# Performance work log

Measured on AMD Instinct MI355X. Metric: run time of the kernel, lower is better.

Reference implementation:

```python
import jax, jax.numpy as jnp
import numpy as np

B, T, V, LSRC, D = 4, 128, 50257, 512, 512
PAD_ID = 0
GAMMA1, GAMMA2 = 1.0, 0.1
BETA, MAX_ITER = 2.0, 400


def setup_inputs() -> dict:
    key = jax.random.key(0)
    ks = jax.random.split(key, 7)
    # output_mle are per-token probabilities (original takes torch.log of them)
    output_mle = jax.random.uniform(ks[0], (B, T, V), jnp.float32, 1e-4, 1.0)
    attn_dist = jax.random.uniform(ks[1], (B, LSRC, T), jnp.float32)
    coverage = jax.random.uniform(ks[2], (B, LSRC, T), jnp.float32)
    trg = jax.random.randint(ks[3], (B, T), 0, V)
    dec_mask = jax.random.randint(ks[4], (B, T), 0, 2).astype(bool)
    dec_len = jax.random.randint(ks[5], (B,), 1, T)
    W_emb = jax.random.normal(ks[6], (V, D), jnp.float32) * 0.02
    return {"output_mle": output_mle, "attn_dist": attn_dist, "coverage": coverage,
            "trg": trg, "dec_mask": dec_mask, "dec_len": dec_len, "W_emb": W_emb}


def ipot(a1, a2, beta=BETA, max_iter=MAX_ITER):
    # a1, a2: [n, d_hid] (already flattened from [B, T, d_hid])
    n = a1.shape[0]
    a1n = a1 / jnp.linalg.norm(a1, axis=1, keepdims=True)
    a2n = a2 / jnp.linalg.norm(a2, axis=1, keepdims=True)
    C = a1n @ a2n.T                      # [n, n] cosine cost
    A = jnp.exp(-C / beta)
    eye = jnp.eye(n, dtype=C.dtype)
    sigma0 = jnp.full((n, 1), 1.0 / n, C.dtype)
    T0 = jnp.full((n, n), 1.0 / (n * n), C.dtype)

    def step(carry, _):
        Tm, sigma = carry
        Q = A * Tm
        dvec = 1.0 / n / (Q @ sigma)          # [n, 1]
        sigma = 1.0 / n / (Q.T @ dvec)        # [n, 1]
        # Faithful to torch source: diag(d) * Q * diag(sigma) is ELEMENTWISE,
        # so only the diagonal of the product survives.
        Tm = dvec * Q * sigma.T * eye
        return (Tm, sigma), None

    (Tm, _), _ = jax.lax.scan(step, (T0, sigma0), None, length=max_iter)
    return jnp.sum(Tm * C)


def reference(output_mle, attn_dist, coverage, trg, dec_mask, dec_len, W_emb):
    # --- NLL loss (Eq. 6): mean -log p[target] over non-pad tokens ---
    logp = jnp.log(output_mle)
    tok_lp = jnp.take_along_axis(logp, trg[..., None], axis=-1)[..., 0]   # [B, T]
    valid = (trg != PAD_ID)
    nll = -jnp.sum(jnp.where(valid, tok_lp, 0.0)) / jnp.sum(valid).astype(logp.dtype)

    # --- Coverage loss (Eq. 12) ---
    cov = jnp.sum(jnp.minimum(attn_dist, coverage), axis=1)               # [B, T]
    cov = jnp.where(dec_mask, 0.0, cov)
    cov_loss = jnp.sum(cov) / jnp.sum(dec_len).astype(cov.dtype)

    # --- OT loss via IPOT ---
    trg_emb = W_emb[trg]                                                  # [B, T, D]
    probs = jax.nn.softmax(output_mle, axis=-1)
    pred = jnp.einsum('btv,vd->btd', probs, W_emb)                        # [B, T, D]
    ot = ipot(pred.reshape(-1, D), trg_emb.reshape(-1, D))

    # Faithful to source: gamma2 added as a constant (not multiplied by ot)
    return nll + GAMMA1 * cov_loss + GAMMA2 + ot
```

## Files before the change

### kernel.cpp

```cpp
#include <hip/hip_runtime.h>
#include <math.h>

#define B_ 4
#define T_ 128
#define V_ 50257
#define D_ 512
#define NROWS 512
#define GAMMA2_ 0.1f

#define BK 32
#define KC 1600
#define SPLITK 32
#define NIT (KC / BK)
#define LDA 40
#define LDB 40

#define SLICE (NROWS * D_)

typedef __attribute__((ext_vector_type(8))) short s8v;
typedef __attribute__((ext_vector_type(4))) float f4v;

#define WS_PART_OFF 1024

__device__ inline unsigned int pack2bf(float f0, float f1) {
    unsigned int u0 = __float_as_uint(f0);
    unsigned int u1 = __float_as_uint(f1);
    u0 += 0x7fffu + ((u0 >> 16) & 1u);
    u1 += 0x7fffu + ((u1 >> 16) & 1u);
    return (u0 >> 16) | (u1 & 0xffff0000u);
}

__device__ inline void sync_lds() {
    __builtin_amdgcn_s_waitcnt(0xC07F);
    __builtin_amdgcn_s_barrier();
}

__device__ inline float wave_reduce(float v) {
    #pragma unroll
    for (int o = 32; o > 0; o >>= 1) v += __shfl_down(v, o, 64);
    return v;
}

__global__ void misc_kernel(const float* __restrict__ output_mle,
                            const float* __restrict__ attn,
                            const float* __restrict__ cover,
                            const int* __restrict__ trg,
                            const int* __restrict__ dec_mask,
                            const int* __restrict__ dec_len,
                            float* __restrict__ acc) {
    int bid = blockIdx.x;
    if (bid < 64) {
        float s = 0.f;
        const float4* a4 = (const float4*)attn;
        const float4* c4 = (const float4*)cover;
        for (int i4 = bid * 256 + threadIdx.x; i4 < 65536; i4 += 64 * 256) {
            float4 a = a4[i4];
            float4 c = c4[i4];
            int b = i4 >> 14;
            int t = (i4 << 2) & (T_ - 1);
            int4 m = *(const int4*)&dec_mask[(b << 7) + t];
            s += m.x ? 0.f : fminf(a.x, c.x);
            s += m.y ? 0.f : fminf(a.y, c.y);
            s += m.z ? 0.f : fminf(a.z, c.z);
            s += m.w ? 0.f : fminf(a.w, c.w);
        }
        s = wave_reduce(s);
        if ((threadIdx.x & 63) == 0) atomicAdd(&acc[2], s);
    } else {
        float lp = 0.f, cnt = 0.f;
        for (int i = threadIdx.x; i < NROWS; i += 256) {
            int tg = trg[i];
            if (tg != 0) {
                lp += __logf(output_mle[(size_t)i * V_ + tg]);
                cnt += 1.f;
            }
        }
        lp = wave_reduce(lp); cnt = wave_reduce(cnt);
        if ((threadIdx.x & 63) == 0) { atomicAdd(&acc[0], lp); atomicAdd(&acc[1], cnt); }
        if (threadIdx.x < B_) atomicAdd(&acc[3], (float)dec_len[threadIdx.x]);
    }
}

__launch_bounds__(256)
__global__ void gemm_kernel(const float* __restrict__ X,
                            const float* __restrict__ W,
                            float* __restrict__ part,
                            int use_atomic) {
    __shared__ __align__(16) short As[128 * LDA];
    __shared__ __align__(16) short Bs[128 * LDB];

    const int bx   = blockIdx.x;
    const int tile = bx & 15;
    const int s    = bx >> 4;
    const int i0   = (tile & 3) * 128;
    const int d0   = (tile >> 2) * 128;
    const int ks   = s * KC;
    const int ke   = min(ks + KC, V_);

    const int tid  = threadIdx.x;
    const int lane = tid & 63;
    const int wave = tid >> 6;
    const int wm   = (wave & 1) * 64;
    const int wn   = (wave >> 1) * 64;
    const int l15  = lane & 15;
    const int l4   = lane >> 4;

    const int ar   = tid >> 1;
    const int akh  = (tid & 1) * 16;
    const int bn2  = (tid & 63) * 2;
    const int bkq  = (tid >> 6) * 8;

    f4v acc[4][4];
    #pragma unroll
    for (int a = 0; a < 4; a++)
        #pragma unroll
        for (int b = 0; b < 4; b++) acc[a][b] = (f4v)0.f;

    auto stageA = [&](const float4 (&ab)[4]) {
        const float* f = (const float*)&ab[0];
        unsigned int au[8];
        #pragma unroll
        for (int p = 0; p < 8; p++)
            au[p] = pack2bf(__expf(f[2 * p]), __expf(f[2 * p + 1]));
        *(uint4*)&As[ar * LDA + akh]     = *(const uint4*)&au[0];
        *(uint4*)&As[ar * LDA + akh + 8] = *(const uint4*)&au[4];
    };
    auto stageB = [&](const float2 (&bb)[8]) {
        unsigned int r0[4], r1[4];
        #pragma unroll
        for (int p = 0; p < 4; p++) {
            r0[p] = pack2bf(bb[2 * p].x, bb[2 * p + 1].x);
            r1[p] = pack2bf(bb[2 * p].y, bb[2 * p + 1].y);
        }
        *(uint4*)&Bs[bn2 * LDB + bkq]       = *(const uint4*)&r0[0];
        *(uint4*)&Bs[(bn2 + 1) * LDB + bkq] = *(const uint4*)&r1[0];
    };
    auto domfma = [&]() {
        s8v af[4], bfr[4];
        #pragma unroll
        for (int mi = 0; mi < 4; mi++)
            af[mi] = *(const s8v*)&As[(wm + mi * 16 + l15) * LDA + l4 * 8];
        #pragma unroll
        for (int ni = 0; ni < 4; ni++)
            bfr[ni] = *(const s8v*)&Bs[(wn + ni * 16 + l15) * LDB + l4 * 8];
        #pragma unroll
        for (int mi = 0; mi < 4; mi++)
            #pragma unroll
            for (int ni = 0; ni < 4; ni++)
                acc[mi][ni] = __builtin_amdgcn_mfma_f32_16x16x32_bf16(
                    af[mi], bfr[ni], acc[mi][ni], 0, 0, 0);
    };
    auto issue = [&](float4 (&ab)[4], float2 (&bb)[8], const float* ap, const float* bp) {
        #pragma unroll
        for (int q = 0; q < 4; q++) ab[q] = *(const float4*)(ap + q * 4);
        #pragma unroll
        for (int j = 0; j < 8; j++) bb[j] = *(const float2*)(bp + (size_t)j * D_);
    };

    if (ks + KC <= V_) {
        const float* ap = X + (size_t)(i0 + ar) * V_ + ks + akh;
        const float* bp = W + d0 + bn2 + (size_t)(ks + bkq) * D_;
        float4 a0[4], a1[4];
        float2 b0[8], b1[8];
        issue(a0, b0, ap, bp);
        #pragma unroll 1
        for (int it = 0; it < NIT; it += 2) {
            ap += BK; bp += (size_t)BK * D_;
            if (it + 1 < NIT) issue(a1, b1, ap, bp);
            sync_lds();
            stageA(a0); stageB(b0);
            sync_lds();
            domfma();

            ap += BK; bp += (size_t)BK * D_;
            if (it + 2 < NIT) issue(a0, b0, ap, bp);
            sync_lds();
            stageA(a1); stageB(b1);
            sync_lds();
            domfma();
        }
    } else {
        const float* Abase = X + (size_t)(i0 + ar) * V_;
        const float* Bbase = W + d0 + bn2;
        for (int k0 = ks; k0 < ke; k0 += BK) {
            float4 ab[4];
            float2 bb[8];
            #pragma unroll
            for (int q = 0; q < 4; q++) {
                int gk = min(k0 + akh + q * 4, V_ - 4);
                ab[q] = *(const float4*)(Abase + gk);
            }
            #pragma unroll
            for (int j = 0; j < 8; j++) {
                int gk = min(k0 + bkq + j, V_ - 1);
                bb[j] = *(const float2*)(Bbase + (size_t)gk * D_);
            }
            sync_lds();
            {
                unsigned int au[8];
                const float* f = (const float*)&ab[0];
                #pragma unroll
                for (int p = 0; p < 8; p++) {
                    int g0 = k0 + akh + 2 * p;
                    float e0 = (g0     < ke) ? __expf(f[2 * p])     : 0.f;
                    float e1 = (g0 + 1 < ke) ? __expf(f[2 * p + 1]) : 0.f;
                    au[p] = pack2bf(e0, e1);
                }
                *(uint4*)&As[ar * LDA + akh]     = *(const uint4*)&au[0];
                *(uint4*)&As[ar * LDA + akh + 8] = *(const uint4*)&au[4];
            }
            {
                unsigned int r0[4], r1[4];
                #pragma unroll
                for (int p = 0; p < 4; p++) {
                    int g0 = k0 + bkq + 2 * p;
                    float x0 = (g0     < ke) ? bb[2 * p].x     : 0.f;
                    float x1 = (g0 + 1 < ke) ? bb[2 * p + 1].x : 0.f;
                    float y0 = (g0     < ke) ? bb[2 * p].y     : 0.f;
                    float y1 = (g0 + 1 < ke) ? bb[2 * p + 1].y : 0.f;
                    r0[p] = pack2bf(x0, x1);
                    r1[p] = pack2bf(y0, y1);
                }
                *(uint4*)&Bs[bn2 * LDB + bkq]       = *(const uint4*)&r0[0];
                *(uint4*)&Bs[(bn2 + 1) * LDB + bkq] = *(const uint4*)&r1[0];
            }
            sync_lds();
            domfma();
        }
    }

    float* dst = part + (use_atomic ? 0 : (size_t)s * SLICE);
    #pragma unroll
    for (int mi = 0; mi < 4; mi++) {
        #pragma unroll
        for (int ni = 0; ni < 4; ni++) {
            int col = d0 + wn + ni * 16 + l15;
            #pragma unroll
            for (int r = 0; r < 4; r++) {
                int row = i0 + wm + mi * 16 + l4 * 4 + r;
                if (use_atomic) atomicAdd(&dst[row * D_ + col], acc[mi][ni][r]);
                else            dst[row * D_ + col] = acc[mi][ni][r];
            }
        }
    }
}

__global__ void ot_kernel(const float* __restrict__ part,
                          const float* __restrict__ W,
                          const int* __restrict__ trg,
                          float* __restrict__ acc,
                          int nsl) {
    int wave = threadIdx.x >> 6, lane = threadIdx.x & 63;
    int row  = blockIdx.x * 4 + wave;
    const size_t off = (size_t)row * D_ + lane * 8;

    float4 p0 = {0, 0, 0, 0}, p1 = {0, 0, 0, 0};
    for (int s = 0; s < nsl; s++) {
        const float4* ps = (const float4*)(part + (size_t)s * SLICE + off);
        float4 q0 = ps[0], q1 = ps[1];
        p0.x += q0.x; p0.y += q0.y; p0.z += q0.z; p0.w += q0.w;
        p1.x += q1.x; p1.y += q1.y; p1.z += q1.z; p1.w += q1.w;
    }
    const float4* t4 = (const float4*)(W + (size_t)trg[row] * D_ + lane * 8);
    float4 t0 = t4[0], t1 = t4[1];

    float dot = p0.x * t0.x + p0.y * t0.y + p0.z * t0.z + p0.w * t0.w
              + p1.x * t1.x + p1.y * t1.y + p1.z * t1.z + p1.w * t1.w;
    float nn  = p0.x * p0.x + p0.y * p0.y + p0.z * p0.z + p0.w * p0.w
              + p1.x * p1.x + p1.y * p1.y + p1.z * p1.z + p1.w * p1.w;
    float tt  = t0.x * t0.x + t0.y * t0.y + t0.z * t0.z + t0.w * t0.w
              + t1.x * t1.x + t1.y * t1.y + t1.z * t1.z + t1.w * t1.w;

    dot = wave_reduce(dot); nn = wave_reduce(nn); tt = wave_reduce(tt);
    if (lane == 0)
        atomicAdd(&acc[4], (dot / sqrtf(nn * tt)) * (1.0f / (float)NROWS));
}

__global__ void finalize_kernel(const float* __restrict__ acc, float* __restrict__ out) {
    if (threadIdx.x == 0)
        out[0] = -acc[0] / acc[1] + acc[2] / acc[3] + GAMMA2_ + acc[4];
}

extern "C" void kernel_launch(void* const* d_in, const int* in_sizes, int n_in,
                              void* d_out, int out_size, void* d_ws, size_t ws_size,
                              hipStream_t stream) {
    const float* output_mle = (const float*)d_in[0];
    const float* attn       = (const float*)d_in[1];
    const float* cover      = (const float*)d_in[2];
    const int*   trg        = (const int*)d_in[3];
    const int*   dec_mask   = (const int*)d_in[4];
    const int*   dec_len    = (const int*)d_in[5];
    const float* W          = (const float*)d_in[6];
    float* out  = (float*)d_out;
    float* acc  = (float*)d_ws;
    float* part = acc + WS_PART_OFF;

    const size_t need = (size_t)WS_PART_OFF * 4 + (size_t)SPLITK * SLICE * 4;
    const bool partial = (ws_size >= need);

    if (partial) {
        hipMemsetAsync(d_ws, 0, WS_PART_OFF * sizeof(float), stream);
    } else {
        hipMemsetAsync(d_ws, 0, (WS_PART_OFF + SLICE) * sizeof(float), stream);
    }
    misc_kernel<<<65, 256, 0, stream>>>(output_mle, attn, cover, trg, dec_mask, dec_len, acc);
    gemm_kernel<<<16 * SPLITK, 256, 0, stream>>>(output_mle, W, part, partial ? 0 : 1);
    ot_kernel<<<NROWS / 4, 256, 0, stream>>>(part, W, trg, acc, partial ? SPLITK : 1);
    finalize_kernel<<<1, 64, 0, stream>>>(acc, out);
}
```

Measured before the change: 322.0 us.

## Pre-convert exp(X) and transposed W to bf16 buffers, then run a direct-to-LDS GEMM

Adds a prep kernel that computes exp of the probabilities and packs them to bf16 in a padded buffer, transposes W into a bf16 K-major buffer, and folds in the misc (NLL/coverage) work. A new GEMM uses global_load_lds to move the bf16 tiles straight into LDS and runs with a 48-way K split. The aim is to remove fp32 loads and in-loop conversion from the GEMM inner loop. In exchange it adds a large extra write and reread of bf16 copies (~50MB each) and needs a much larger workspace, falling back to the old path otherwise.

```diff
diff --git a/kernel.cpp b/kernel.cpp
--- a/kernel.cpp
+++ b/kernel.cpp
@@ -14,13 +14,22 @@
 #define NIT (KC / BK)
 #define LDA 40
 #define LDB 40
-
 #define SLICE (NROWS * D_)
+#define WS_PART_OFF 1024
+
+#define SPLITK2 48
+#define KC2 1056
+#define KP 50688
+#define NXB 2048
+#define NWB ((KP / 64) * (D_ / 64))
+#define ACC_BYTES 4096
+#define XB_BYTES ((size_t)NROWS * KP * 2)
+#define WT_BYTES ((size_t)D_ * KP * 2)
+#define PART2_BYTES ((size_t)SPLITK2 * SLICE * 4)
+#define NEED_NEW (ACC_BYTES + XB_BYTES + WT_BYTES + PART2_BYTES)
 
 typedef __attribute__((ext_vector_type(8))) short s8v;
 typedef __attribute__((ext_vector_type(4))) float f4v;
-
-#define WS_PART_OFF 1024
 
 __device__ inline unsigned int pack2bf(float f0, float f1) {
     unsigned int u0 = __float_as_uint(f0);
@@ -41,14 +50,20 @@
     return v;
 }
 
-__global__ void misc_kernel(const float* __restrict__ output_mle,
-                            const float* __restrict__ attn,
-                            const float* __restrict__ cover,
-                            const int* __restrict__ trg,
-                            const int* __restrict__ dec_mask,
-                            const int* __restrict__ dec_len,
-                            float* __restrict__ acc) {
-    int bid = blockIdx.x;
+__device__ __forceinline__ void gload16(const unsigned short* g, unsigned short* l) {
+    __builtin_amdgcn_global_load_lds(
+        (const __attribute__((address_space(1))) unsigned int*)g,
+        (__attribute__((address_space(3))) unsigned int*)l, 16, 0, 0);
+}
+
+__device__ void misc_body(int bid,
+                          const float* __restrict__ output_mle,
+                          const float* __restrict__ attn,
+                          const float* __restrict__ cover,
+                          const int* __restrict__ trg,
+                          const int* __restrict__ dec_mask,
+                          const int* __restrict__ dec_len,
+                          float* __restrict__ acc) {
     if (bid < 64) {
         float s = 0.f;
         const float4* a4 = (const float4*)attn;
@@ -81,6 +96,159 @@
     }
 }
 
+__global__ void misc_kernel(const float* __restrict__ output_mle,
+                            const float* __restrict__ attn,
+                            const float* __restrict__ cover,
+                            const int* __restrict__ trg,
+                            const int* __restrict__ dec_mask,
+                            const int* __restrict__ dec_len,
+                            float* __restrict__ acc) {
+    misc_body(blockIdx.x, output_mle, attn, cover, trg, dec_mask, dec_len, acc);
+}
+
+__launch_bounds__(256)
+__global__ void prep_kernel(const float* __restrict__ X,
+                            const float* __restrict__ W,
+                            const float* __restrict__ attn,
+                            const float* __restrict__ cover,
+                            const int* __restrict__ trg,
+                            const int* __restrict__ dec_mask,
+                            const int* __restrict__ dec_len,
+                            float* __restrict__ acc,
+                            unsigned short* __restrict__ Xb,
+                            unsigned short* __restrict__ Wt) {
+    const int bid = blockIdx.x;
+    const int tid = threadIdx.x;
+    if (bid < NXB) {
+        const int upr = KP / 8;
+        for (int u = bid * 256 + tid; u < NROWS * upr; u += NXB * 256) {
+            int row = u / upr;
+            int k8  = (u - row * upr) * 8;
+            const float* src = X + (size_t)row * V_ + k8;
+            unsigned int pk[4];
+            if (k8 + 8 <= V_) {
+                float e[8];
+                #pragma unroll
+                for (int j = 0; j < 8; j++) e[j] = __expf(src[j]);
+                #pragma unroll
+                for (int p = 0; p < 4; p++) pk[p] = pack2bf(e[2 * p], e[2 * p + 1]);
+            } else {
+                #pragma unroll
+                for (int p = 0; p < 4; p++) {
+                    float e0 = (k8 + 2 * p     < V_) ? __expf(src[2 * p])     : 0.f;
+                    float e1 = (k8 + 2 * p + 1 < V_) ? __expf(src[2 * p + 1]) : 0.f;
+                    pk[p] = pack2bf(e0, e1);
+                }
+            }
+            *(uint4*)&Xb[(size_t)row * KP + k8] = *(uint4*)pk;
+        }
+    } else if (bid < NXB + NWB) {
+        __shared__ float Ls[64][64];
+        int w  = bid - NXB;
+        int kt = w >> 3;
+        int dt = w & 7;
+        int k0 = kt << 6, d0 = dt << 6;
+        int r0 = tid >> 4;
+        int c0 = (tid & 15) << 2;
+        #pragma unroll
+        for (int q = 0; q < 4; q++) {
+            int r  = (q << 4) + r0;
+            int gk = k0 + r;
+            float4 v;
+            if (gk < V_) v = *(const float4*)&W[(size_t)gk * D_ + d0 + c0];
+            else         v = make_float4(0.f, 0.f, 0.f, 0.f);
+            *(float4*)&Ls[r][c0] = v;
+        }
+        __syncthreads();
+        int d  = tid >> 2;
+        int kc = (tid & 3) << 4;
+        unsigned int pk[8];
+        #pragma unroll
+        for (int p = 0; p < 8; p++)
+            pk[p] = pack2bf(Ls[kc + 2 * p][d], Ls[kc + 2 * p + 1][d]);
+        unsigned short* dst = Wt + (size_t)(d0 + d) * KP + k0 + kc;
+        *(uint4*)&dst[0] = *(uint4*)&pk[0];
+        *(uint4*)&dst[8] = *(uint4*)&pk[4];
+    } else {
+        misc_body(bid - (NXB + NWB), X, attn, cover, trg, dec_mask, dec_len, acc);
+    }
+}
+
+__launch_bounds__(256)
+__global__ void gemm2_kernel(const unsigned short* __restrict__ Xb,
+                             const unsigned short* __restrict__ Wt,
+                             float* __restrict__ part) {
+    __shared__ __align__(16) unsigned short As[128 * 32];
+    __shared__ __align__(16) unsigned short Bs[128 * 32];
+
+    const int bx   = blockIdx.x;
+    const int tile = bx & 15;
+    const int s    = bx >> 4;
+    const int i0   = (tile & 3) * 128;
+    const int d0   = (tile >> 2) * 128;
+    const size_t ks = (size_t)s * KC2;
+
+    const int tid  = threadIdx.x;
+    const int lane = tid & 63;
+    const int wave = tid >> 6;
+    const int wm   = (wave & 1) * 64;
+    const int wn   = (wave >> 1) * 64;
+    const int l15  = lane & 15;
+    const int l4   = lane >> 4;
+
+    const int grow = wave * 16 + (lane >> 2);
+    const int gk8  = (lane & 3) * 8;
+    const unsigned short* gA0 = Xb + (size_t)(i0 + grow) * KP + ks + gk8;
+    const unsigned short* gA1 = gA0 + (size_t)64 * KP;
+    const unsigned short* gB0 = Wt + (size_t)(d0 + grow) * KP + ks + gk8;
+    const unsigned short* gB1 = gB0 + (size_t)64 * KP;
+    unsigned short* lA = As + wave * 512;
+    unsigned short* lB = Bs + wave * 512;
+
+    f4v acc[4][4];
+    #pragma unroll
+    for (int a = 0; a < 4; a++)
+        #pragma unroll
+        for (int b = 0; b < 4; b++) acc[a][b] = (f4v)0.f;
+
+    #pragma unroll 1
+    for (int kk = 0; kk < KC2; kk += 32) {
+        __syncthreads();
+        gload16(gA0 + kk, lA);
+        gload16(gA1 + kk, lA + 2048);
+        gload16(gB0 + kk, lB);
+        gload16(gB1 + kk, lB + 2048);
+        __syncthreads();
+        s8v af[4], bfr[4];
+        #pragma unroll
+        for (int mi = 0; mi < 4; mi++)
+            af[mi] = *(const s8v*)&As[(wm + mi * 16 + l15) * 32 + l4 * 8];
+        #pragma unroll
+        for (int ni = 0; ni < 4; ni++)
+            bfr[ni] = *(const s8v*)&Bs[(wn + ni * 16 + l15) * 32 + l4 * 8];
+        #pragma unroll
+        for (int mi = 0; mi < 4; mi++)
+            #pragma unroll
+            for (int ni = 0; ni < 4; ni++)
+                acc[mi][ni] = __builtin_amdgcn_mfma_f32_16x16x32_bf16(
+                    af[mi], bfr[ni], acc[mi][ni], 0, 0, 0);
+    }
+
+    float* dst = part + (size_t)s * SLICE;
+    #pragma unroll
+    for (int mi = 0; mi < 4; mi++) {
+        #pragma unroll
+        for (int ni = 0; ni < 4; ni++) {
+            int col = d0 + wn + ni * 16 + l15;
+            #pragma unroll
+            for (int r = 0; r < 4; r++) {
+                int row = i0 + wm + mi * 16 + l4 * 4 + r;
+                dst[row * D_ + col] = acc[mi][ni][r];
+            }
+        }
+    }
+}
+
 __launch_bounds__(256)
 __global__ void gemm_kernel(const float* __restrict__ X,
                             const float* __restrict__ W,
@@ -293,18 +461,31 @@
     const float* W          = (const float*)d_in[6];
     float* out  = (float*)d_out;
     float* acc  = (float*)d_ws;
-    float* part = acc + WS_PART_OFF;
-
-    const size_t need = (size_t)WS_PART_OFF * 4 + (size_t)SPLITK * SLICE * 4;
-    const bool partial = (ws_size >= need);
-
-    if (partial) {
-        hipMemsetAsync(d_ws, 0, WS_PART_OFF * sizeof(float), stream);
+
+    const bool newpath = (ws_size >= NEED_NEW);
+
+    if (newpath) {
+        unsigned short* Xb = (unsigned short*)((char*)d_ws + ACC_BYTES);
+        unsigned short* Wt = (unsigned short*)((char*)d_ws + ACC_BYTES + XB_BYTES);
+        float* part2 = (float*)((char*)d_ws + ACC_BYTES + XB_BYTES + WT_BYTES);
+        hipMemsetAsync(d_ws, 0, ACC_BYTES, stream);
+        prep_kernel<<<NXB + NWB + 65, 256, 0, stream>>>(
+            output_mle, W, attn, cover, trg, dec_mask, dec_len, acc, Xb, Wt);
+        gemm2_kernel<<<16 * SPLITK2, 256, 0, stream>>>(Xb, Wt, part2);
+        ot_kernel<<<NROWS / 4, 256, 0, stream>>>(part2, W, trg, acc, SPLITK2);
+        finalize_kernel<<<1, 64, 0, stream>>>(acc, out);
     } else {
-        hipMemsetAsync(d_ws, 0, (WS_PART_OFF + SLICE) * sizeof(float), stream);
-    }
-    misc_kernel<<<65, 256, 0, stream>>>(output_mle, attn, cover, trg, dec_mask, dec_len, acc);
-    gemm_kernel<<<16 * SPLITK, 256, 0, stream>>>(output_mle, W, part, partial ? 0 : 1);
-    ot_kernel<<<NROWS / 4, 256, 0, stream>>>(part, W, trg, acc, partial ? SPLITK : 1);
-    finalize_kernel<<<1, 64, 0, stream>>>(acc, out);
-}
+        float* part = acc + WS_PART_OFF;
+        const size_t need = (size_t)WS_PART_OFF * 4 + (size_t)SPLITK * SLICE * 4;
+        const bool partial = (ws_size >= need);
+        if (partial) {
+            hipMemsetAsync(d_ws, 0, WS_PART_OFF * sizeof(float), stream);
+        } else {
+            hipMemsetAsync(d_ws, 0, (WS_PART_OFF + SLICE) * sizeof(float), stream);
+        }
+        misc_kernel<<<65, 256, 0, stream>>>(output_mle, attn, cover, trg, dec_mask, dec_len, acc);
+        gemm_kernel<<<16 * SPLITK, 256, 0, stream>>>(output_mle, W, part, partial ? 0 : 1);
+        ot_kernel<<<NROWS / 4, 256, 0, stream>>>(part, W, trg, acc, partial ? SPLITK : 1);
+        finalize_kernel<<<1, 64, 0, stream>>>(acc, out);
+    }
+}
```

After: 331.0 us. 1.03x slower.

## Group GEMM split-K blocks by XCD and parallelize OT partial reduction

Applied to the files above, without the earlier changes.

Remaps GEMM block indices so that all 16 output tiles sharing one K-slice land on the same XCD, letting them share the W slice in that XCD's L2. The OT kernel now uses one block per row, with four waves each summing a quarter of the split-K partials; the wave results are combined through shared memory. This aims to cut L2 misses in the GEMM and raise memory-level parallelism in the partial-sum reduction. The cost is 4x more OT blocks plus an extra LDS barrier.

```diff
diff --git a/kernel.cpp b/kernel.cpp
--- a/kernel.cpp
+++ b/kernel.cpp
@@ -90,8 +90,10 @@
     __shared__ __align__(16) short Bs[128 * LDB];
 
     const int bx   = blockIdx.x;
-    const int tile = bx & 15;
-    const int s    = bx >> 4;
+    const int xcd  = bx & 7;
+    const int j    = bx >> 3;
+    const int s    = xcd + 8 * (j >> 4);
+    const int tile = j & 15;
     const int i0   = (tile & 3) * 128;
     const int d0   = (tile >> 2) * 128;
     const int ks   = s * KC;
@@ -154,7 +156,7 @@
         #pragma unroll
         for (int q = 0; q < 4; q++) ab[q] = *(const float4*)(ap + q * 4);
         #pragma unroll
-        for (int j = 0; j < 8; j++) bb[j] = *(const float2*)(bp + (size_t)j * D_);
+        for (int j2 = 0; j2 < 8; j2++) bb[j2] = *(const float2*)(bp + (size_t)j2 * D_);
     };
 
     if (ks + KC <= V_) {
@@ -191,9 +193,9 @@
                 ab[q] = *(const float4*)(Abase + gk);
             }
             #pragma unroll
-            for (int j = 0; j < 8; j++) {
-                int gk = min(k0 + bkq + j, V_ - 1);
-                bb[j] = *(const float2*)(Bbase + (size_t)gk * D_);
+            for (int j2 = 0; j2 < 8; j2++) {
+                int gk = min(k0 + bkq + j2, V_ - 1);
+                bb[j2] = *(const float2*)(Bbase + (size_t)gk * D_);
             }
             sync_lds();
             {
@@ -250,30 +252,44 @@
                           const int* __restrict__ trg,
                           float* __restrict__ acc,
                           int nsl) {
+    __shared__ float Ps[4][D_];
     int wave = threadIdx.x >> 6, lane = threadIdx.x & 63;
-    int row  = blockIdx.x * 4 + wave;
+    int row  = blockIdx.x;
     const size_t off = (size_t)row * D_ + lane * 8;
 
     float4 p0 = {0, 0, 0, 0}, p1 = {0, 0, 0, 0};
-    for (int s = 0; s < nsl; s++) {
+    for (int s = wave; s < nsl; s += 4) {
         const float4* ps = (const float4*)(part + (size_t)s * SLICE + off);
         float4 q0 = ps[0], q1 = ps[1];
         p0.x += q0.x; p0.y += q0.y; p0.z += q0.z; p0.w += q0.w;
         p1.x += q1.x; p1.y += q1.y; p1.z += q1.z; p1.w += q1.w;
     }
-    const float4* t4 = (const float4*)(W + (size_t)trg[row] * D_ + lane * 8);
-    float4 t0 = t4[0], t1 = t4[1];
-
-    float dot = p0.x * t0.x + p0.y * t0.y + p0.z * t0.z + p0.w * t0.w
-              + p1.x * t1.x + p1.y * t1.y + p1.z * t1.z + p1.w * t1.w;
-    float nn  = p0.x * p0.x + p0.y * p0.y + p0.z * p0.z + p0.w * p0.w
-              + p1.x * p1.x + p1.y * p1.y + p1.z * p1.z + p1.w * p1.w;
-    float tt  = t0.x * t0.x + t0.y * t0.y + t0.z * t0.z + t0.w * t0.w
-              + t1.x * t1.x + t1.y * t1.y + t1.z * t1.z + t1.w * t1.w;
-
-    dot = wave_reduce(dot); nn = wave_reduce(nn); tt = wave_reduce(tt);
-    if (lane == 0)
-        atomicAdd(&acc[4], (dot / sqrtf(nn * tt)) * (1.0f / (float)NROWS));
+    *(float4*)&Ps[wave][lane * 8]     = p0;
+    *(float4*)&Ps[wave][lane * 8 + 4] = p1;
+    __syncthreads();
+    if (wave == 0) {
+        float4 s0 = {0, 0, 0, 0}, s1 = {0, 0, 0, 0};
+        #pragma unroll
+        for (int w = 0; w < 4; w++) {
+            float4 q0 = *(const float4*)&Ps[w][lane * 8];
+            float4 q1 = *(const float4*)&Ps[w][lane * 8 + 4];
+            s0.x += q0.x; s0.y += q0.y; s0.z += q0.z; s0.w += q0.w;
+            s1.x += q1.x; s1.y += q1.y; s1.z += q1.z; s1.w += q1.w;
+        }
+        const float4* t4 = (const float4*)(W + (size_t)trg[row] * D_ + lane * 8);
+        float4 t0 = t4[0], t1 = t4[1];
+
+        float dot = s0.x * t0.x + s0.y * t0.y + s0.z * t0.z + s0.w * t0.w
+                  + s1.x * t1.x + s1.y * t1.y + s1.z * t1.z + s1.w * t1.w;
+        float nn  = s0.x * s0.x + s0.y * s0.y + s0.z * s0.z + s0.w * s0.w
+                  + s1.x * s1.x + s1.y * s1.y + s1.z * s1.z + s1.w * s1.w;
+        float tt  = t0.x * t0.x + t0.y * t0.y + t0.z * t0.z + t0.w * t0.w
+                  + t1.x * t1.x + t1.y * t1.y + t1.z * t1.z + t1.w * t1.w;
+
+        dot = wave_reduce(dot); nn = wave_reduce(nn); tt = wave_reduce(tt);
+        if (lane == 0)
+            atomicAdd(&acc[4], (dot / sqrtf(nn * tt)) * (1.0f / (float)NROWS));
+    }
 }
 
 __global__ void finalize_kernel(const float* __restrict__ acc, float* __restrict__ out) {
@@ -305,6 +321,6 @@
     }
     misc_kernel<<<65, 256, 0, stream>>>(output_mle, attn, cover, trg, dec_mask, dec_len, acc);
     gemm_kernel<<<16 * SPLITK, 256, 0, stream>>>(output_mle, W, part, partial ? 0 : 1);
-    ot_kernel<<<NROWS / 4, 256, 0, stream>>>(part, W, trg, acc, partial ? SPLITK : 1);
+    ot_kernel<<<NROWS, 256, 0, stream>>>(part, W, trg, acc, partial ? SPLITK : 1);
     finalize_kernel<<<1, 64, 0, stream>>>(acc, out);
 }
```

Measured after the change: 315.5 us. -2.0%, faster.
